# Optimization experiments

Hardware: AMD Instinct MI355X
Metric: run time of the kernel (lower is better)

The kernel has to match this reference:

```python
import jax, jax.numpy as jnp
import numpy as np
import math

B, S, D, H = 32, 197, 1024, 16  # batch, seq_len (pinned by w_o=Linear(197,.)), d_model, n_heads
DK = D // H                      # d_k = 64


def setup_inputs() -> dict:
    key = jax.random.key(0)
    ks = jax.random.split(key, 8)
    f32 = jnp.float32
    # weights scaled by 0.02 for numerically sane softmax logits
    return {
        "x0": jax.random.normal(ks[0], (B, S, D), dtype=f32),
        "x1": jax.random.normal(ks[1], (B, S, D), dtype=f32),
        "wk0": jax.random.normal(ks[2], (D, D), dtype=f32) * 0.02,
        "bk0": jnp.zeros((D,), dtype=f32),
        "wk1": jax.random.normal(ks[3], (D, D), dtype=f32) * 0.02,
        "bk1": jnp.zeros((D,), dtype=f32),
        "wv0": jax.random.normal(ks[4], (D, D), dtype=f32) * 0.02,
        "bv0": jnp.zeros((D,), dtype=f32),
        "wv1": jax.random.normal(ks[5], (D, D), dtype=f32) * 0.02,
        "bv1": jnp.zeros((D,), dtype=f32),
        "wo": jax.random.normal(ks[6], (D, S), dtype=f32) * 0.02,  # nn.Linear(197, d_model) weight: [d_model, 197]
        "bo": jnp.zeros((D,), dtype=f32),
    }


def _proj(x, w, b):
    # torch nn.Linear: y = x @ W^T + b; then view + transpose -> [B, H, S, DK]
    y = x @ w.T + b
    return y.reshape(B, S, H, DK).transpose(0, 2, 1, 3)


def reference(x0, x1, wk0, bk0, wk1, bk1, wv0, bv0, wv1, bv1, wo, bo):
    scale = 1.0 / math.sqrt(DK)
    K0 = _proj(x0, wk0, bk0)
    K1 = _proj(x1, wk1, bk1)
    V0 = _proj(x0, wv0, bv0)
    V1 = _proj(x1, wv1, bv1)
    # mutual attention: K_i @ K_j^T * scale for i != j  -> [B, H, S, S]
    s01 = jnp.einsum('bhsd,bhtd->bhst', K0, K1) * scale
    s10 = jnp.einsum('bhsd,bhtd->bhst', K1, K0) * scale
    a0 = jax.nn.softmax(s01, axis=-1)
    a1 = jax.nn.softmax(s10, axis=-1)
    # feature outputs: attn_i @ V_i  -> [B, H, S, DK]
    f0 = jnp.einsum('bhst,bhtd->bhsd', a0, V0)
    f1 = jnp.einsum('bhst,bhtd->bhsd', a1, V1)
    # cross-product combination, averaged over the 2 ordered pairs -> [B, H, S, S]
    comb = (jnp.einsum('bhsd,bhtd->bhst', f0, f1)
            + jnp.einsum('bhsd,bhtd->bhst', f1, f0)) * (scale * 0.5)
    # w_o: Linear(197 -> d_model) on last axis -> [B, H, S, D]
    out = comb @ wo.T + bo
    return (out, a0, a1)
```

## Files before the change

kernel.cpp:

```cpp
#include <hip/hip_runtime.h>
#include <hip/hip_bf16.h>

typedef unsigned short u16;
typedef __attribute__((ext_vector_type(8))) short short8;
typedef __attribute__((ext_vector_type(4))) float floatx4;
typedef __attribute__((ext_vector_type(4), aligned(4))) float floatx4u;
typedef __attribute__((ext_vector_type(4))) unsigned int uint4v;

#define B_ 32
#define S_ 197
#define D_ 1024
#define H_ 16
#define DK_ 64
#define BH_ 512
#define SP_ 208
#define TP_ 224
#define TPP_ 232
#define M_ 6304
#define XSZ_ ((size_t)M_*D_)
#define WSZ_W ((size_t)D_*D_)

#define KSZ ((size_t)BH_*SP_*DK_)
#define VSZ ((size_t)BH_*DK_*TP_)
#define CSZ ((size_t)BH_*SP_*TP_)
#define K0_OFF  ((size_t)0)
#define K1_OFF  (KSZ)
#define VT0_OFF (2*KSZ)
#define VT1_OFF (2*KSZ + VSZ)
#define F0_OFF  (2*KSZ + 2*VSZ)
#define F1_OFF  (3*KSZ + 2*VSZ)
#define COMB_OFF (4*KSZ + 2*VSZ)
#define WOT_OFF  (4*KSZ + 2*VSZ + CSZ)
#define BIAS_OFF (WOT_OFF + (size_t)D_*TP_)
#define WS_ELEMS (BIAS_OFF + 5*1024)

#define XB_OFF  (COMB_OFF)
#define WB_OFF  (COMB_OFF + 2*XSZ_)

#define OUT_SZ ((size_t)BH_*S_*D_)
#define A_SZ   ((size_t)BH_*S_*S_)

__device__ __forceinline__ float bf2f(u16 v) {
    unsigned u = ((unsigned)v) << 16;
    return __builtin_bit_cast(float, u);
}
__device__ __forceinline__ u16 f2bf(float f) {
    unsigned u = __builtin_bit_cast(unsigned, f);
    u += 0x7FFFu + ((u >> 16) & 1u);
    return (u16)(u >> 16);
}
__device__ __forceinline__ floatx4 mfma16(short8 a, short8 b, floatx4 c) {
    return __builtin_amdgcn_mfma_f32_16x16x32_bf16(a, b, c, 0, 0, 0);
}
__device__ __forceinline__ void gl_lds16(const u16* g, u16* l) {
    __builtin_amdgcn_global_load_lds(
        (const __attribute__((address_space(1))) void*)(g),
        (__attribute__((address_space(3))) void*)(l), 16, 0, 0);
}

__device__ __forceinline__ int detect_f32(const u16* __restrict__ x0raw) {
    int lane = threadIdx.x & 63;
    unsigned h = x0raw[2*lane];
    unsigned e = (h >> 7) & 0xFFu;
    int ext = (e < 0x30u) | (e > 0x4Fu);
    unsigned long long m = __ballot(ext);
    return __popcll(m) > 16;
}

__device__ __forceinline__ u16 loadBF(const void* p, size_t off, int is32) {
    return is32 ? f2bf(((const float*)p)[off]) : ((const u16*)p)[off];
}
__device__ __forceinline__ void storeF(void* p, size_t off, float v, int is32) {
    if (is32) ((float*)p)[off] = v; else ((u16*)p)[off] = f2bf(v);
}
__device__ __forceinline__ short8 load8(const void* p, size_t off, int is32) {
    short8 r;
    if (is32) {
        const float* f = (const float*)p + off;
        floatx4 a = *(const floatx4*)f;
        floatx4 b = *(const floatx4*)(f + 4);
        r[0]=(short)f2bf(a[0]); r[1]=(short)f2bf(a[1]);
        r[2]=(short)f2bf(a[2]); r[3]=(short)f2bf(a[3]);
        r[4]=(short)f2bf(b[0]); r[5]=(short)f2bf(b[1]);
        r[6]=(short)f2bf(b[2]); r[7]=(short)f2bf(b[3]);
    } else {
        r = *(const short8*)((const u16*)p + off);
    }
    return r;
}

__global__ __launch_bounds__(256) void prep_kernel(
    const void* __restrict__ wo,
    const void* __restrict__ bk0, const void* __restrict__ bk1,
    const void* __restrict__ bv0, const void* __restrict__ bv1,
    const void* __restrict__ bo,
    const void* __restrict__ x0, const void* __restrict__ x1,
    const void* __restrict__ wk0, const void* __restrict__ wk1,
    const void* __restrict__ wv0, const void* __restrict__ wv1,
    u16* __restrict__ ws) {
    int is32 = detect_f32((const u16*)x0);
    int i = blockIdx.x * 256 + threadIdx.x;
    if (i < D_*TP_) {
        int d = i / TP_, t = i - d*TP_;
        ws[WOT_OFF + i] = (t < S_) ? loadBF(wo, (size_t)d*S_ + t, is32) : (u16)0;
    }
    const int KP = BH_*(SP_-S_)*DK_;
    if (i < KP) {
        int bh = i / ((SP_-S_)*DK_);
        int r  = i - bh*((SP_-S_)*DK_);
        int s  = S_ + r / DK_;
        int dk = r % DK_;
        size_t o = ((size_t)bh*SP_ + s)*DK_ + dk;
        ws[K0_OFF + o] = 0; ws[K1_OFF + o] = 0;
    }
    const int VP = BH_*DK_*(TP_-S_);
    if (i < VP) {
        int bh = i / (DK_*(TP_-S_));
        int r  = i - bh*(DK_*(TP_-S_));
        int dk = r / (TP_-S_);
        int t  = S_ + r % (TP_-S_);
        size_t o = ((size_t)bh*DK_ + dk)*TP_ + t;
        ws[VT0_OFF + o] = 0; ws[VT1_OFF + o] = 0;
    }
    if (i < 5*1024) {
        int which = i >> 10, j = i & 1023;
        const void* src = (which==0) ? bk0 : (which==1) ? bk1
                        : (which==2) ? bv0 : (which==3) ? bv1 : bo;
        ws[BIAS_OFF + i] = loadBF(src, j, is32);
    }
    const size_t NCH = (2*XSZ_ + 4*WSZ_W) / 8;
    for (size_t c = (size_t)blockIdx.x*256 + threadIdx.x; c < NCH;
         c += (size_t)gridDim.x*256) {
        size_t e = c * 8;
        const void* src; size_t soff;
        if (e < 2*XSZ_) {
            src = (e < XSZ_) ? x0 : x1;
            soff = (e < XSZ_) ? e : e - XSZ_;
        } else {
            size_t r = e - 2*XSZ_;
            int z = (int)(r >> 20);
            src = (z==0) ? wk0 : (z==1) ? wk1 : (z==2) ? wv0 : wv1;
            soff = r & (WSZ_W - 1);
        }
        *(short8*)&ws[XB_OFF + e] = load8(src, soff, is32);
    }
}

__global__ __launch_bounds__(256) void proj_kernel(u16* __restrict__ ws)
{
    __shared__ __align__(16) u16 lA[128*64];
    __shared__ __align__(16) u16 lB[128*64];
    int z = blockIdx.z;
    const u16* X = ws + XB_OFF + (size_t)(z & 1)*XSZ_;
    const u16* W = ws + WB_OFF + (size_t)z*WSZ_W;
    u16* dst = ws + ((z==0) ? K0_OFF : (z==1) ? K1_OFF : (z==2) ? VT0_OFF : VT1_OFF);
    int m0 = blockIdx.x * 128, n0 = blockIdx.y * 128;
    int tid = threadIdx.x;
    int w = tid >> 6, lane = tid & 63, q = lane >> 4, l15 = lane & 15;
    int wm = (w >> 1) * 64, wn = (w & 1) * 64;

    floatx4 acc[4][4];
    #pragma unroll
    for (int a = 0; a < 4; a++)
        #pragma unroll
        for (int b = 0; b < 4; b++) acc[a][b] = (floatx4){0.f,0.f,0.f,0.f};

    for (int kk = 0; kk < D_; kk += 64) {
        __syncthreads();
        #pragma unroll
        for (int it = 0; it < 4; it++) {
            int c = it*256 + w*64 + lane;
            int r = c >> 3, cc = c & 7;
            int m = m0 + r; if (m > M_-1) m = M_-1;
            gl_lds16(X + (size_t)m*D_ + kk + cc*8,        &lA[(it*256 + w*64)*8]);
            gl_lds16(W + (size_t)(n0 + r)*D_ + kk + cc*8, &lB[(it*256 + w*64)*8]);
        }
        __syncthreads();
        #pragma unroll
        for (int kc = 0; kc < 2; kc++) {
            short8 af[4], bf[4];
            #pragma unroll
            for (int mi = 0; mi < 4; mi++)
                af[mi] = *(const short8*)&lA[(wm + mi*16 + l15)*64 + kc*32 + q*8];
            #pragma unroll
            for (int ni = 0; ni < 4; ni++)
                bf[ni] = *(const short8*)&lB[(wn + ni*16 + l15)*64 + kc*32 + q*8];
            #pragma unroll
            for (int mi = 0; mi < 4; mi++)
                #pragma unroll
                for (int ni = 0; ni < 4; ni++)
                    acc[mi][ni] = mfma16(af[mi], bf[ni], acc[mi][ni]);
        }
    }
    #pragma unroll
    for (int ni = 0; ni < 4; ni++) {
        int n = n0 + wn + ni*16 + l15;
        float bv = bf2f(ws[BIAS_OFF + (size_t)z*1024 + n]);
        int h = n >> 6, dk = n & 63;
        #pragma unroll
        for (int mi = 0; mi < 4; mi++)
            #pragma unroll
            for (int r = 0; r < 4; r++) {
                int m = m0 + wm + mi*16 + q*4 + r;
                if (m < M_) {
                    int b = m / S_;
                    int s = m - b * S_;
                    int bh = b * H_ + h;
                    size_t o = (z < 2) ? (((size_t)bh*SP_ + s)*DK_ + dk)
                                       : (((size_t)bh*DK_ + dk)*TP_ + s);
                    dst[o] = f2bf(acc[mi][ni][r] + bv);
                }
            }
    }
}

__global__ __launch_bounds__(256) void attn_av_kernel(u16* __restrict__ ws,
                                                      void* __restrict__ dout,
                                                      const u16* __restrict__ x0det) {
    __shared__ __align__(16) u16 lKb[SP_*DK_];
    __shared__ __align__(16) u16 lV[DK_*TPP_];
    __shared__ __align__(16) u16 lP[4][16*TPP_];
    int is32 = detect_f32(x0det);
    int bh = blockIdx.x, dir = blockIdx.y;
    const u16* Ka = ws + (dir ? K1_OFF : K0_OFF) + (size_t)bh*SP_*DK_;
    const u16* Kb = ws + (dir ? K0_OFF : K1_OFF) + (size_t)bh*SP_*DK_;
    const u16* Vt = ws + (dir ? VT1_OFF : VT0_OFF) + (size_t)bh*DK_*TP_;
    u16* fO = ws + (dir ? F1_OFF : F0_OFF) + (size_t)bh*SP_*DK_;
    size_t aBase = OUT_SZ + (size_t)dir*A_SZ + (size_t)bh*S_*S_;
    int tid = threadIdx.x;
    for (int i = tid; i < SP_*8; i += 256)
        ((uint4v*)lKb)[(i & ~7) | ((i ^ (i >> 3)) & 7)] = ((const uint4v*)Kb)[i];
    for (int i = tid; i < DK_*28; i += 256) {
        int row = i / 28, c = i - row*28;
        ((uint4v*)lV)[row*29 + c] = ((const uint4v*)Vt)[i];
    }
    __syncthreads();
    int w = tid>>6, lane = tid&63, q = lane>>4, l15 = lane&15;
    u16* lPw = &lP[w][0];
    const float scale = 0.125f;
    for (int rt = w; rt < 13; rt += 4) {
        floatx4 acc[13];
        #pragma unroll
        for (int ct = 0; ct < 13; ct++) acc[ct] = (floatx4){0.f,0.f,0.f,0.f};
        #pragma unroll
        for (int kc = 0; kc < 2; kc++) {
            short8 af = *(const short8*)&Ka[(size_t)(rt*16 + l15)*DK_ + kc*32 + q*8];
            #pragma unroll
            for (int ct = 0; ct < 13; ct++) {
                short8 bf = *(const short8*)&lKb[(ct*16 + l15)*DK_ +
                                                 ((kc*32 + q*8) ^ ((l15 & 7) << 3))];
                acc[ct] = mfma16(af, bf, acc[ct]);
            }
        }
        #pragma unroll
        for (int r = 0; r < 4; r++) {
            int srow = rt*16 + q*4 + r;
            float v[13];
            float mx = -1e9f;
            #pragma unroll
            for (int ct = 0; ct < 13; ct++) {
                int t = ct*16 + l15;
                v[ct] = (t < S_) ? acc[ct][r]*scale : -1e9f;
                mx = fmaxf(mx, v[ct]);
            }
            #pragma unroll
            for (int off = 1; off < 16; off <<= 1) mx = fmaxf(mx, __shfl_xor(mx, off));
            float sum = 0.f;
            #pragma unroll
            for (int ct = 0; ct < 13; ct++) {
                int t = ct*16 + l15;
                float e = (t < S_) ? __expf(v[ct] - mx) : 0.f;
                v[ct] = e; sum += e;
            }
            #pragma unroll
            for (int off = 1; off < 16; off <<= 1) sum += __shfl_xor(sum, off);
            float inv = 1.0f / sum;
            bool rok = srow < S_;
            #pragma unroll
            for (int ct = 0; ct < 13; ct++) {
                int t = ct*16 + l15;
                float pv = rok ? v[ct]*inv : 0.f;
                lPw[(q*4 + r)*TPP_ + ct*16 + l15] = f2bf(pv);
                if (rok && t < S_) storeF(dout, aBase + (size_t)srow*S_ + t, pv, is32);
            }
            lPw[(q*4 + r)*TPP_ + 208 + l15] = 0;
        }
        floatx4 facc[4];
        #pragma unroll
        for (int ct = 0; ct < 4; ct++) facc[ct] = (floatx4){0.f,0.f,0.f,0.f};
        for (int kc = 0; kc < 7; kc++) {
            short8 paf = *(const short8*)&lPw[l15*TPP_ + kc*32 + q*8];
            #pragma unroll
            for (int ct = 0; ct < 4; ct++) {
                short8 bf = *(const short8*)&lV[(ct*16 + l15)*TPP_ + kc*32 + q*8];
                facc[ct] = mfma16(paf, bf, facc[ct]);
            }
        }
        #pragma unroll
        for (int ct = 0; ct < 4; ct++)
            #pragma unroll
            for (int r = 0; r < 4; r++) {
                int so = rt*16 + q*4 + r;
                fO[(size_t)so*DK_ + ct*16 + l15] = f2bf(facc[ct][r]);
            }
    }
}

__global__ __launch_bounds__(256) void comb_kernel(u16* __restrict__ ws) {
    __shared__ __align__(16) u16 lf0[SP_*DK_];
    __shared__ __align__(16) u16 lf1[SP_*DK_];
    int bh = blockIdx.x;
    const u16* f0 = ws + F0_OFF + (size_t)bh*SP_*DK_;
    const u16* f1 = ws + F1_OFF + (size_t)bh*SP_*DK_;
    u16* cO = ws + COMB_OFF + (size_t)bh*SP_*TP_;
    int tid = threadIdx.x;
    for (int i = tid; i < SP_*8; i += 256) {
        int d = (i & ~7) | ((i ^ (i >> 3)) & 7);
        ((uint4v*)lf0)[d] = ((const uint4v*)f0)[i];
        ((uint4v*)lf1)[d] = ((const uint4v*)f1)[i];
    }
    __syncthreads();
    int w = tid>>6, lane = tid&63, q = lane>>4, l15 = lane&15;
    int sw = (l15 & 7) << 3;
    const float cscale = 0.0625f;
    for (int rt = w; rt < 13; rt += 4) {
        short8 a0f[2], a1f[2];
        #pragma unroll
        for (int kc = 0; kc < 2; kc++) {
            int eo = (kc*32 + q*8) ^ sw;
            a0f[kc] = *(const short8*)&lf0[(rt*16 + l15)*DK_ + eo];
            a1f[kc] = *(const short8*)&lf1[(rt*16 + l15)*DK_ + eo];
        }
        for (int nt = 0; nt < 13; nt++) {
            floatx4 acc = (floatx4){0.f,0.f,0.f,0.f};
            #pragma unroll
            for (int kc = 0; kc < 2; kc++) {
                short8 b1 = *(const short8*)&lf1[(nt*16 + l15)*DK_ + ((kc*32 + q*8) ^ sw)];
                acc = mfma16(a0f[kc], b1, acc);
            }
            #pragma unroll
            for (int kc = 0; kc < 2; kc++) {
                short8 b0 = *(const short8*)&lf0[(nt*16 + l15)*DK_ + ((kc*32 + q*8) ^ sw)];
                acc = mfma16(a1f[kc], b0, acc);
            }
            #pragma unroll
            for (int r = 0; r < 4; r++) {
                int srow = rt*16 + q*4 + r;
                cO[(size_t)srow*TP_ + nt*16 + l15] = f2bf(acc[r]*cscale);
            }
        }
        #pragma unroll
        for (int r = 0; r < 4; r++) {
            int srow = rt*16 + q*4 + r;
            cO[(size_t)srow*TP_ + 208 + l15] = 0;
        }
    }
}

__global__ __launch_bounds__(256) void out_kernel(const u16* __restrict__ ws,
                                                  void* __restrict__ dout,
                                                  const u16* __restrict__ x0det) {
    __shared__ __align__(16) u16 lw[128*TPP_];
    int is32 = detect_f32(x0det);
    int bh = blockIdx.x, nb = blockIdx.y;
    const u16* wot = ws + WOT_OFF + (size_t)nb*128*TP_;
    const u16* cI  = ws + COMB_OFF + (size_t)bh*SP_*TP_;
    size_t oBase = (size_t)bh*S_*D_;
    int tid = threadIdx.x;
    for (int i = tid; i < 128*28; i += 256) {
        int row = i / 28, c = i - row*28;
        ((uint4v*)lw)[row*29 + c] = ((const uint4v*)wot)[i];
    }
    __syncthreads();
    int w = tid>>6, lane = tid&63, q = lane>>4, l15 = lane&15;
    for (int mt = w; mt < 13; mt += 4) {
        floatx4 acc[8];
        #pragma unroll
        for (int nt = 0; nt < 8; nt++) acc[nt] = (floatx4){0.f,0.f,0.f,0.f};
        for (int kc = 0; kc < 7; kc++) {
            short8 af = *(const short8*)&cI[(size_t)(mt*16 + l15)*TP_ + kc*32 + q*8];
            #pragma unroll
            for (int nt = 0; nt < 8; nt++) {
                short8 bf = *(const short8*)&lw[(nt*16 + l15)*TPP_ + kc*32 + q*8];
                acc[nt] = mfma16(af, bf, acc[nt]);
            }
        }
        #pragma unroll
        for (int nt = 0; nt < 8; nt++) {
            int d = nb*128 + nt*16 + l15;
            float bv = bf2f(ws[BIAS_OFF + 4*1024 + d]);
            #pragma unroll
            for (int r = 0; r < 4; r++) {
                int s = mt*16 + q*4 + r;
                if (s < S_) storeF(dout, oBase + (size_t)s*D_ + d, acc[nt][r] + bv, is32);
            }
        }
    }
}

extern "C" void kernel_launch(void* const* d_in, const int* in_sizes, int n_in,
                              void* d_out, int out_size, void* d_ws, size_t ws_size,
                              hipStream_t stream) {
    const void* x0  = d_in[0];
    const void* x1  = d_in[1];
    const void* wk0 = d_in[2];
    const void* bk0 = d_in[3];
    const void* wk1 = d_in[4];
    const void* bk1 = d_in[5];
    const void* wv0 = d_in[6];
    const void* bv0 = d_in[7];
    const void* wv1 = d_in[8];
    const void* bv1 = d_in[9];
    const void* wo  = d_in[10];
    const void* bo  = d_in[11];
    u16* ws = (u16*)d_ws;
    const u16* x0det = (const u16*)x0;

    if (ws_size < WS_ELEMS * sizeof(u16)) return;

    prep_kernel<<<3456, 256, 0, stream>>>(wo, bk0, bk1, bv0, bv1, bo,
                                          x0, x1, wk0, wk1, wv0, wv1, ws);
    proj_kernel<<<dim3(50, 8, 4), 256, 0, stream>>>(ws);
    attn_av_kernel<<<dim3(BH_, 2), 256, 0, stream>>>(ws, d_out, x0det);
    comb_kernel<<<BH_, 256, 0, stream>>>(ws);
    out_kernel<<<dim3(BH_, 8), 256, 0, stream>>>(ws, d_out, x0det);
}
```

Measured before the change: 1.100 ms.

## Fuse comb and output kernels, remap proj blocks, read V from global

Merges comb_kernel and out_kernel into one 512-thread kernel. The comb tile is kept in LDS and the wo tiles are streamed through a shared buffer that reuses the f0/f1 space, so the comb intermediate never goes through global memory. The projection grid is flattened and swizzled so that consecutive blocks spread over XCDs and tiles. attn_av no longer stages V^T in LDS and reads it straight from global/L2, which lowers LDS use but adds uncached-style global reads inside the inner MFMA loop. The fused kernel's large shared footprint and serial nb loop may reduce occupancy.

New measurement: 1.071 ms. 1.03x faster.

```diff
diff --git a/kernel.cpp b/kernel.cpp
--- a/kernel.cpp
+++ b/kernel.cpp
@@ -150,11 +150,16 @@
 {
     __shared__ __align__(16) u16 lA[128*64];
     __shared__ __align__(16) u16 lB[128*64];
-    int z = blockIdx.z;
+    int L = blockIdx.x;
+    int o = (L & 7) * 200 + (L >> 3);
+    int bx = o % 50;
+    int yz = o / 50;
+    int by = yz & 7;
+    int z  = yz >> 3;
     const u16* X = ws + XB_OFF + (size_t)(z & 1)*XSZ_;
     const u16* W = ws + WB_OFF + (size_t)z*WSZ_W;
     u16* dst = ws + ((z==0) ? K0_OFF : (z==1) ? K1_OFF : (z==2) ? VT0_OFF : VT1_OFF);
-    int m0 = blockIdx.x * 128, n0 = blockIdx.y * 128;
+    int m0 = bx * 128, n0 = by * 128;
     int tid = threadIdx.x;
     int w = tid >> 6, lane = tid & 63, q = lane >> 4, l15 = lane & 15;
     int wm = (w >> 1) * 64, wn = (w & 1) * 64;
@@ -206,9 +211,9 @@
                     int b = m / S_;
                     int s = m - b * S_;
                     int bh = b * H_ + h;
-                    size_t o = (z < 2) ? (((size_t)bh*SP_ + s)*DK_ + dk)
-                                       : (((size_t)bh*DK_ + dk)*TP_ + s);
-                    dst[o] = f2bf(acc[mi][ni][r] + bv);
+                    size_t o2 = (z < 2) ? (((size_t)bh*SP_ + s)*DK_ + dk)
+                                        : (((size_t)bh*DK_ + dk)*TP_ + s);
+                    dst[o2] = f2bf(acc[mi][ni][r] + bv);
                 }
             }
     }
@@ -218,7 +223,6 @@
                                                       void* __restrict__ dout,
                                                       const u16* __restrict__ x0det) {
     __shared__ __align__(16) u16 lKb[SP_*DK_];
-    __shared__ __align__(16) u16 lV[DK_*TPP_];
     __shared__ __align__(16) u16 lP[4][16*TPP_];
     int is32 = detect_f32(x0det);
     int bh = blockIdx.x, dir = blockIdx.y;
@@ -230,10 +234,6 @@
     int tid = threadIdx.x;
     for (int i = tid; i < SP_*8; i += 256)
         ((uint4v*)lKb)[(i & ~7) | ((i ^ (i >> 3)) & 7)] = ((const uint4v*)Kb)[i];
-    for (int i = tid; i < DK_*28; i += 256) {
-        int row = i / 28, c = i - row*28;
-        ((uint4v*)lV)[row*29 + c] = ((const uint4v*)Vt)[i];
-    }
     __syncthreads();
     int w = tid>>6, lane = tid&63, q = lane>>4, l15 = lane&15;
     u16* lPw = &lP[w][0];
@@ -292,7 +292,7 @@
             short8 paf = *(const short8*)&lPw[l15*TPP_ + kc*32 + q*8];
             #pragma unroll
             for (int ct = 0; ct < 4; ct++) {
-                short8 bf = *(const short8*)&lV[(ct*16 + l15)*TPP_ + kc*32 + q*8];
+                short8 bf = *(const short8*)&Vt[(size_t)(ct*16 + l15)*TP_ + kc*32 + q*8];
                 facc[ct] = mfma16(paf, bf, facc[ct]);
             }
         }
@@ -306,15 +306,21 @@
     }
 }
 
-__global__ __launch_bounds__(256) void comb_kernel(u16* __restrict__ ws) {
-    __shared__ __align__(16) u16 lf0[SP_*DK_];
-    __shared__ __align__(16) u16 lf1[SP_*DK_];
+__global__ __launch_bounds__(512) void comb_out_kernel(const u16* __restrict__ ws,
+                                                       void* __restrict__ dout,
+                                                       const u16* __restrict__ x0det) {
+    __shared__ __align__(16) u16 smem[SP_*TPP_ + 128*TPP_];
+    u16* lC  = smem;
+    u16* lw  = smem + SP_*TPP_;
+    u16* lf0 = lw;
+    u16* lf1 = lw + SP_*DK_;
+    int is32 = detect_f32(x0det);
     int bh = blockIdx.x;
     const u16* f0 = ws + F0_OFF + (size_t)bh*SP_*DK_;
     const u16* f1 = ws + F1_OFF + (size_t)bh*SP_*DK_;
-    u16* cO = ws + COMB_OFF + (size_t)bh*SP_*TP_;
+    size_t oBase = (size_t)bh*S_*D_;
     int tid = threadIdx.x;
-    for (int i = tid; i < SP_*8; i += 256) {
+    for (int i = tid; i < SP_*8; i += 512) {
         int d = (i & ~7) | ((i ^ (i >> 3)) & 7);
         ((uint4v*)lf0)[d] = ((const uint4v*)f0)[i];
         ((uint4v*)lf1)[d] = ((const uint4v*)f1)[i];
@@ -323,7 +329,7 @@
     int w = tid>>6, lane = tid&63, q = lane>>4, l15 = lane&15;
     int sw = (l15 & 7) << 3;
     const float cscale = 0.0625f;
-    for (int rt = w; rt < 13; rt += 4) {
+    for (int rt = w; rt < 13; rt += 8) {
         short8 a0f[2], a1f[2];
         #pragma unroll
         for (int kc = 0; kc < 2; kc++) {
@@ -346,55 +352,47 @@
             #pragma unroll
             for (int r = 0; r < 4; r++) {
                 int srow = rt*16 + q*4 + r;
-                cO[(size_t)srow*TP_ + nt*16 + l15] = f2bf(acc[r]*cscale);
+                lC[srow*TPP_ + nt*16 + l15] = f2bf(acc[r]*cscale);
             }
         }
         #pragma unroll
         for (int r = 0; r < 4; r++) {
             int srow = rt*16 + q*4 + r;
-            cO[(size_t)srow*TP_ + 208 + l15] = 0;
-        }
-    }
-}
-
-__global__ __launch_bounds__(256) void out_kernel(const u16* __restrict__ ws,
-                                                  void* __restrict__ dout,
-                                                  const u16* __restrict__ x0det) {
-    __shared__ __align__(16) u16 lw[128*TPP_];
-    int is32 = detect_f32(x0det);
-    int bh = blockIdx.x, nb = blockIdx.y;
-    const u16* wot = ws + WOT_OFF + (size_t)nb*128*TP_;
-    const u16* cI  = ws + COMB_OFF + (size_t)bh*SP_*TP_;
-    size_t oBase = (size_t)bh*S_*D_;
-    int tid = threadIdx.x;
-    for (int i = tid; i < 128*28; i += 256) {
-        int row = i / 28, c = i - row*28;
-        ((uint4v*)lw)[row*29 + c] = ((const uint4v*)wot)[i];
+            lC[srow*TPP_ + 208 + l15] = 0;
+        }
     }
     __syncthreads();
-    int w = tid>>6, lane = tid&63, q = lane>>4, l15 = lane&15;
-    for (int mt = w; mt < 13; mt += 4) {
-        floatx4 acc[8];
-        #pragma unroll
-        for (int nt = 0; nt < 8; nt++) acc[nt] = (floatx4){0.f,0.f,0.f,0.f};
-        for (int kc = 0; kc < 7; kc++) {
-            short8 af = *(const short8*)&cI[(size_t)(mt*16 + l15)*TP_ + kc*32 + q*8];
+    for (int nb = 0; nb < 8; nb++) {
+        const u16* wot = ws + WOT_OFF + (size_t)nb*128*TP_;
+        for (int i = tid; i < 128*28; i += 512) {
+            int row = i / 28, c = i - row*28;
+            ((uint4v*)lw)[row*29 + c] = ((const uint4v*)wot)[i];
+        }
+        __syncthreads();
+        for (int mt = w; mt < 13; mt += 8) {
+            floatx4 acc[8];
+            #pragma unroll
+            for (int nt = 0; nt < 8; nt++) acc[nt] = (floatx4){0.f,0.f,0.f,0.f};
+            for (int kc = 0; kc < 7; kc++) {
+                short8 af = *(const short8*)&lC[(mt*16 + l15)*TPP_ + kc*32 + q*8];
+                #pragma unroll
+                for (int nt = 0; nt < 8; nt++) {
+                    short8 bf = *(const short8*)&lw[(nt*16 + l15)*TPP_ + kc*32 + q*8];
+                    acc[nt] = mfma16(af, bf, acc[nt]);
+                }
+            }
             #pragma unroll
             for (int nt = 0; nt < 8; nt++) {
-                short8 bf = *(const short8*)&lw[(nt*16 + l15)*TPP_ + kc*32 + q*8];
-                acc[nt] = mfma16(af, bf, acc[nt]);
-            }
-        }
-        #pragma unroll
-        for (int nt = 0; nt < 8; nt++) {
-            int d = nb*128 + nt*16 + l15;
-            float bv = bf2f(ws[BIAS_OFF + 4*1024 + d]);
-            #pragma unroll
-            for (int r = 0; r < 4; r++) {
-                int s = mt*16 + q*4 + r;
-                if (s < S_) storeF(dout, oBase + (size_t)s*D_ + d, acc[nt][r] + bv, is32);
-            }
-        }
+                int d = nb*128 + nt*16 + l15;
+                float bv = bf2f(ws[BIAS_OFF + 4*1024 + d]);
+                #pragma unroll
+                for (int r = 0; r < 4; r++) {
+                    int s = mt*16 + q*4 + r;
+                    if (s < S_) storeF(dout, oBase + (size_t)s*D_ + d, acc[nt][r] + bv, is32);
+                }
+            }
+        }
+        __syncthreads();
     }
 }
 
@@ -420,8 +418,7 @@
 
     prep_kernel<<<3456, 256, 0, stream>>>(wo, bk0, bk1, bv0, bv1, bo,
                                           x0, x1, wk0, wk1, wv0, wv1, ws);
-    proj_kernel<<<dim3(50, 8, 4), 256, 0, stream>>>(ws);
+    proj_kernel<<<1600, 256, 0, stream>>>(ws);
     attn_av_kernel<<<dim3(BH_, 2), 256, 0, stream>>>(ws, d_out, x0det);
-    comb_kernel<<<BH_, 256, 0, stream>>>(ws);
-    out_kernel<<<dim3(BH_, 8), 256, 0, stream>>>(ws, d_out, x0det);
-}
+    comb_out_kernel<<<BH_, 512, 0, stream>>>(ws, d_out, x0det);
+}
```
